# Kernel optimization log

Hardware: AMD Instinct MI355X
Metric: run time of the kernel (lower is better)

## Reference

```python
import jax, jax.numpy as jnp
import numpy as np

B, S, D, H = 2, 2048, 1024, 16
HD = D // H  # 64
ROPE_BASE = 10000.0


def setup_inputs() -> dict:
    key = jax.random.key(0)
    k1, k2, k3 = jax.random.split(key, 3)
    std = 1.0 / np.sqrt(D)
    x = jax.random.normal(k1, (B, S, D), dtype=jnp.float32)
    w_in = jax.random.normal(k2, (3 * D, D), dtype=jnp.float32) * std
    w_out = jax.random.normal(k3, (D, D), dtype=jnp.float32) * (std / np.sqrt(2.0))
    return {"x": x, "w_in": w_in, "w_out": w_out}


def _rope_cos_sin(seq_len, head_dim):
    inv_freq = 1.0 / (ROPE_BASE ** (jnp.arange(0, head_dim, 2, dtype=jnp.float32) / head_dim))
    t = jnp.arange(seq_len, dtype=jnp.float32)
    freqs = jnp.einsum("s,d->sd", t, inv_freq)          # [S, HD/2]
    emb = jnp.concatenate([freqs, freqs], axis=-1)       # [S, HD]
    return jnp.cos(emb)[None, :, None, :], jnp.sin(emb)[None, :, None, :]


def _rotate_half(x):
    x1, x2 = jnp.split(x, 2, axis=-1)
    return jnp.concatenate([-x2, x1], axis=-1)


def _apply_rope(x, cos, sin):
    return x * cos + _rotate_half(x) * sin


def reference(x, w_in, w_out):
    b, s, d = x.shape
    # fused QKV projection (no bias)
    qkv = x @ w_in.T                                      # [B, S, 3D]
    q, k, v = jnp.split(qkv, 3, axis=-1)
    q = q.reshape(b, s, H, HD)
    k = k.reshape(b, s, H, HD)
    v = v.reshape(b, s, H, HD)
    # rotary (offset = 0, no KV cache)
    cos, sin = _rope_cos_sin(s, HD)
    q = _apply_rope(q, cos, sin)
    k = _apply_rope(k, cos, sin)
    # causal SDPA, scale 1/sqrt(head_dim)
    scale = 1.0 / jnp.sqrt(jnp.asarray(HD, dtype=x.dtype))
    scores = jnp.einsum("bqhd,bkhd->bhqk", q, k) * scale  # [B, H, S, S]
    causal = jnp.tril(jnp.ones((s, s), dtype=bool))
    scores = jnp.where(causal, scores, jnp.asarray(-jnp.inf, dtype=scores.dtype))
    attn = jax.nn.softmax(scores, axis=-1)
    out = jnp.einsum("bhqk,bkhd->bqhd", attn, v).reshape(b, s, d)
    return out @ w_out.T
```

## Files before the change

kernel.cpp:

```cpp
#include <hip/hip_runtime.h>
#include <hip/hip_bf16.h>
#include <math.h>

#define NB 2
#define NS 2048
#define ND 1024
#define NH 16
#define HD 64
#define BS (NB*NS)
#define D3 (3*ND)
#define NT (NS/64)

typedef __bf16 bf16;
typedef __bf16 bf16x4 __attribute__((ext_vector_type(4)));
typedef __bf16 bf16x8 __attribute__((ext_vector_type(8)));
typedef float f32x4 __attribute__((ext_vector_type(4)));

#define MFMA16(a,b,c) __builtin_amdgcn_mfma_f32_16x16x32_bf16(a,b,c,0,0,0)

static __device__ inline f32x4 zero4() { f32x4 z; z[0]=0.f; z[1]=0.f; z[2]=0.f; z[3]=0.f; return z; }

__device__ __forceinline__ void gload_lds16(const bf16* g, bf16* l) {
    __builtin_amdgcn_global_load_lds(
        (__attribute__((address_space(1))) unsigned int*)g,
        (__attribute__((address_space(3))) unsigned int*)l, 16, 0, 0);
}

#define CVT1 (BS*ND/8)
#define CVT2 (D3*ND/8)
#define CVT3 (ND*ND/8)
#define CVTN (CVT1+CVT2+CVT3)
__global__ __launch_bounds__(256) void prep(
    const float* __restrict__ x, const float* __restrict__ w_in, const float* __restrict__ w_out,
    bf16* __restrict__ xb, bf16* __restrict__ winb, bf16* __restrict__ woutb,
    float* __restrict__ cosT, float* __restrict__ sinT)
{
    int i = blockIdx.x * 256 + threadIdx.x;
    if (i < CVTN) {
        const float* in; bf16* out; int j;
        if (i < CVT1)            { in = x;     out = xb;    j = i; }
        else if (i < CVT1+CVT2)  { in = w_in;  out = winb;  j = i - CVT1; }
        else                     { in = w_out; out = woutb; j = i - CVT1 - CVT2; }
        const float4* p = (const float4*)in;
        float4 a = p[j*2], b = p[j*2+1];
        bf16x8 o;
        o[0]=(bf16)a.x; o[1]=(bf16)a.y; o[2]=(bf16)a.z; o[3]=(bf16)a.w;
        o[4]=(bf16)b.x; o[5]=(bf16)b.y; o[6]=(bf16)b.z; o[7]=(bf16)b.w;
        ((bf16x8*)out)[j] = o;
    } else {
        int k = i - CVTN;
        int s = k >> 5, j = k & 31;
        float inv = __expf(-(float)j * (9.210340372f * 0.03125f));
        float ang = (float)s * inv;
        cosT[k] = cosf(ang);
        sinT[k] = sinf(ang);
    }
}

template<int EPI>
__global__ __launch_bounds__(256) void gemm_bt(
    const bf16* __restrict__ A, const bf16* __restrict__ Bm,
    float* __restrict__ C, bf16* __restrict__ Qb, bf16* __restrict__ Kb, bf16* __restrict__ Vt,
    const float* __restrict__ cosT, const float* __restrict__ sinT,
    int M, int N, int K)
{
    __shared__ bf16 As[2][128*64];
    __shared__ bf16 Bs[2][128*64];
    int t = threadIdx.x;
    int lane = t & 63, w = t >> 6;
    int wr = w >> 1, wc = w & 1;
    int lr = lane & 15, lg = lane >> 4;
    int m0 = blockIdx.y * 128, n0 = blockIdx.x * 128;

    int srow = lane >> 3;
    int schunk = (lane & 7) ^ srow;
    const bf16* gA = &A [(size_t)(m0 + w*32 + srow)*K + schunk*8];
    const bf16* gB = &Bm[(size_t)(n0 + w*32 + srow)*K + schunk*8];

    auto stage = [&](int kt) {
        int buf = kt & 1;
        bf16* lA = &As[buf][w*2048];
        bf16* lB = &Bs[buf][w*2048];
        int k0 = kt * 64;
        #pragma unroll
        for (int i=0;i<4;i++) {
            gload_lds16(gA + (size_t)(i*8)*K + k0, lA + i*512);
            gload_lds16(gB + (size_t)(i*8)*K + k0, lB + i*512);
        }
    };

    f32x4 acc[4][4];
    for (int m=0;m<4;m++) for (int n=0;n<4;n++) acc[m][n] = zero4();

    int nt = K >> 6;
    stage(0);
    stage(1);

    for (int kt = 0; kt < nt; kt++) {
        int cur = kt & 1;
        if (kt < nt-1) asm volatile("s_waitcnt vmcnt(8)" ::: "memory");
        else           asm volatile("s_waitcnt vmcnt(0)" ::: "memory");
        __builtin_amdgcn_s_barrier();
        __builtin_amdgcn_sched_barrier(0);

        bf16x8 af[2][4], bfr[2][4];
        #pragma unroll
        for (int ks=0;ks<2;ks++) {
            #pragma unroll
            for (int m=0;m<4;m++) {
                int row = wr*64 + m*16 + lr;
                af[ks][m] = *(const bf16x8*)&As[cur][row*64 + (((ks*4+lg) ^ (row&7))*8)];
            }
            #pragma unroll
            for (int n=0;n<4;n++) {
                int row = wc*64 + n*16 + lr;
                bfr[ks][n] = *(const bf16x8*)&Bs[cur][row*64 + (((ks*4+lg) ^ (row&7))*8)];
            }
        }
        asm volatile("s_waitcnt lgkmcnt(0)" ::: "memory");
        __builtin_amdgcn_sched_barrier(0);
        __builtin_amdgcn_s_barrier();
        __builtin_amdgcn_sched_barrier(0);

        if (kt + 2 < nt) stage(kt + 2);

        __builtin_amdgcn_s_setprio(1);
        #pragma unroll
        for (int ks=0;ks<2;ks++)
            #pragma unroll
            for (int m=0;m<4;m++)
                #pragma unroll
                for (int n=0;n<4;n++)
                    acc[m][n] = MFMA16(af[ks][m], bfr[ks][n], acc[m][n]);
        __builtin_amdgcn_s_setprio(0);
    }

    if (EPI == 0) {
        for (int m=0;m<4;m++) for (int n=0;n<4;n++) {
            int grow = m0 + wr*64 + m*16 + lg*4;
            int gcol = n0 + wc*64 + n*16 + lr;
            for (int r=0;r<4;r++)
                C[(size_t)(grow+r) * N + gcol] = acc[m][n][r];
        }
    } else {
        int which = n0 >> 10;
        if (which == 2) {
            for (int m=0;m<4;m++) for (int n=0;n<4;n++) {
                int grow = m0 + wr*64 + m*16 + lg*4;
                int gcol = n0 + wc*64 + n*16 + lr;
                int h = (gcol & 1023) >> 6, d = gcol & 63;
                int b = grow >> 11, s0 = grow & (NS-1);
                int shi = s0 & ~63, j = s0 & 63;
                int kp = ((j>>5)&1)*32 + ((j>>2)&3)*8 + ((j>>4)&1)*4;
                bf16x4 pv;
                for (int r=0;r<4;r++) pv[r] = (bf16)acc[m][n][r];
                *(bf16x4*)&Vt[((size_t)((b*NH + h)*HD + d))*NS + shi + kp] = pv;
            }
        } else {
            const float qs = 0.125f * 1.44269504f;
            bf16* dst = (which == 0) ? Qb : Kb;
            for (int m=0;m<4;m++) {
                int grow = m0 + wr*64 + m*16 + lg*4;
                #pragma unroll
                for (int n=0;n<2;n++) {
                    int gcol = n0 + wc*64 + n*16 + lr;
                    int h = (gcol & 1023) >> 6, j = gcol & 63;
                    #pragma unroll
                    for (int r=0;r<4;r++) {
                        int gm = grow + r;
                        int b = gm >> 11, s = gm & (NS-1);
                        float c  = cosT[(s<<5)+j];
                        float sn = sinT[(s<<5)+j];
                        float x1 = acc[m][n][r], x2 = acc[m][n+2][r];
                        float y1 = x1*c - x2*sn;
                        float y2 = x2*c + x1*sn;
                        if (which == 0) { y1 *= qs; y2 *= qs; }
                        size_t off = ((size_t)((b*NH + h)*NS + s))*HD;
                        dst[off + j]      = (bf16)y1;
                        dst[off + j + 32] = (bf16)y2;
                    }
                }
            }
        }
    }
}

__global__ __launch_bounds__(256, 4) void attn_fwd(
    const bf16* __restrict__ Qb, const bf16* __restrict__ Kb, const bf16* __restrict__ Vp,
    bf16* __restrict__ AO)
{
    __shared__ bf16 Ks[2][64*64];
    __shared__ bf16 Vs[2][64*64];
    int t = threadIdx.x;
    int lane = t & 63, w = t >> 6;
    int lr = lane & 15, lg = lane >> 4;
    int wgid = blockIdx.x;
    int qt = (NT-1) - (wgid >> 5);
    int bh = wgid & 31;
    int b = bh >> 4, h = bh & 15;
    size_t base = (size_t)bh * NS * HD;
    int q0 = qt*64 + w*16;

    bf16x8 qf[2];
    #pragma unroll
    for (int c=0;c<2;c++)
        qf[c] = *(const bf16x8*)&Qb[base + (size_t)(q0+lr)*HD + c*32 + lg*8];

    float m_r = -__builtin_inff(), l_r = 0.f;
    f32x4 o[4];
    #pragma unroll
    for (int n=0;n<4;n++) o[n] = zero4();

    int srow = t >> 3;
    int sch  = t & 7;
    int sslot = sch ^ (srow & 7);
    bf16x8 kr[2], vr[2];

    auto load_window = [&](int kv0) {
        #pragma unroll
        for (int i=0;i<2;i++)
            kr[i] = *(const bf16x8*)&Kb[base + (size_t)(kv0 + i*32 + srow)*HD + sch*8];
        #pragma unroll
        for (int i=0;i<2;i++)
            vr[i] = *(const bf16x8*)&Vp[base + (size_t)(i*32 + srow)*NS + kv0 + sch*8];
    };
    auto store_window = [&](int buf) {
        #pragma unroll
        for (int i=0;i<2;i++)
            *(bf16x8*)&Ks[buf][(i*32 + srow)*64 + sslot*8] = kr[i];
        #pragma unroll
        for (int i=0;i<2;i++)
            *(bf16x8*)&Vs[buf][(i*32 + srow)*64 + sslot*8] = vr[i];
    };

    for (int kt = 0; kt <= qt; kt++) {
        if (kt == 0) { load_window(0); store_window(0); __syncthreads(); }
        int cur = kt & 1;
        int kv0 = kt*64;
        bool last = (kt == qt);
        if (!last) load_window(kv0 + 64);

        const bf16* ksb = &Ks[cur][0];
        const bf16* vsb = &Vs[cur][0];

        f32x4 sc[4];
        __builtin_amdgcn_s_setprio(1);
        #pragma unroll
        for (int kb=0;kb<4;kb++) {
            int row = kb*16 + lr;
            bf16x8 k0 = *(const bf16x8*)&ksb[row*64 + ((lg     ^ (row&7))*8)];
            bf16x8 k1 = *(const bf16x8*)&ksb[row*64 + (((4+lg) ^ (row&7))*8)];
            sc[kb] = MFMA16(k0, qf[0], zero4());
            sc[kb] = MFMA16(k1, qf[1], sc[kb]);
        }
        __builtin_amdgcn_s_setprio(0);

        if (last) {
            int qi = q0 + lr;
            #pragma unroll
            for (int kb=0;kb<4;kb++)
                #pragma unroll
                for (int r=0;r<4;r++)
                    if (kv0 + kb*16 + lg*4 + r > qi) sc[kb][r] = -__builtin_inff();
        }

        float tm = fmaxf(fmaxf(sc[0][0],sc[0][1]), fmaxf(sc[0][2],sc[0][3]));
        #pragma unroll
        for (int kb=1;kb<4;kb++)
            tm = fmaxf(tm, fmaxf(fmaxf(sc[kb][0],sc[kb][1]), fmaxf(sc[kb][2],sc[kb][3])));
        tm = fmaxf(tm, __shfl_xor(tm, 16));
        tm = fmaxf(tm, __shfl_xor(tm, 32));
        if (!__all(tm <= m_r + 8.0f)) {
            float mn = fmaxf(m_r, tm);
            float fsc = exp2f(m_r - mn);
            l_r *= fsc;
            #pragma unroll
            for (int n=0;n<4;n++) o[n] *= fsc;
            m_r = mn;
        }
        float p[4][4];
        float ps = 0.f;
        #pragma unroll
        for (int kb=0;kb<4;kb++)
            #pragma unroll
            for (int r=0;r<4;r++) {
                float pe = exp2f(sc[kb][r] - m_r);
                p[kb][r] = pe;
                ps += pe;
            }
        ps += __shfl_xor(ps, 16);
        ps += __shfl_xor(ps, 32);
        l_r += ps;

        bf16x8 pa[2];
        #pragma unroll
        for (int c=0;c<2;c++) {
            bf16x8 v;
            #pragma unroll
            for (int i=0;i<8;i++) v[i] = (bf16)p[c*2 + (i>>2)][i&3];
            pa[c] = v;
        }

        __builtin_amdgcn_s_setprio(1);
        #pragma unroll
        for (int c=0;c<2;c++)
            #pragma unroll
            for (int n=0;n<4;n++) {
                int row = n*16 + lr;
                bf16x8 vf = *(const bf16x8*)&vsb[row*64 + (((c*4+lg) ^ (row&7))*8)];
                o[n] = MFMA16(vf, pa[c], o[n]);
            }
        __builtin_amdgcn_s_setprio(0);

        if (!last) { store_window(cur^1); __syncthreads(); }
    }

    float inv = 1.0f / l_r;
    int q = q0 + lr;
    #pragma unroll
    for (int n=0;n<4;n++) {
        bf16x4 ov;
        #pragma unroll
        for (int r=0;r<4;r++) ov[r] = (bf16)(o[n][r] * inv);
        *(bf16x4*)&AO[((size_t)(b*NS + q)*NH + h)*HD + n*16 + lg*4] = ov;
    }
}

extern "C" void kernel_launch(void* const* d_in, const int* in_sizes, int n_in,
                              void* d_out, int out_size, void* d_ws, size_t ws_size,
                              hipStream_t stream) {
    const float* x     = (const float*)d_in[0];
    const float* w_in  = (const float*)d_in[1];
    const float* w_out = (const float*)d_in[2];
    float* out = (float*)d_out;

    char* p = (char*)d_ws;
    bf16* xb    = (bf16*)p; p += (size_t)BS*ND*2;
    bf16* winb  = (bf16*)p; p += (size_t)D3*ND*2;
    bf16* woutb = (bf16*)p; p += (size_t)ND*ND*2;
    bf16* Qb    = (bf16*)p; p += (size_t)NB*NH*NS*HD*2;
    bf16* Kb    = (bf16*)p; p += (size_t)NB*NH*NS*HD*2;
    bf16* Vp    = (bf16*)p; p += (size_t)NB*NH*NS*HD*2;
    bf16* AO    = (bf16*)p; p += (size_t)BS*ND*2;
    float* cosT = (float*)p; p += (size_t)NS*32*4;
    float* sinT = (float*)p; p += (size_t)NS*32*4;

    prep<<<(CVTN + NS*32)/256, 256, 0, stream>>>(x, w_in, w_out, xb, winb, woutb, cosT, sinT);
    gemm_bt<1><<<dim3(D3/128, BS/128), 256, 0, stream>>>(xb, winb, nullptr, Qb, Kb, Vp,
                                                         cosT, sinT, BS, D3, ND);
    attn_fwd<<<NB*NH*NT, 256, 0, stream>>>(Qb, Kb, Vp, AO);
    gemm_bt<0><<<dim3(ND/128, BS/128), 256, 0, stream>>>(AO, woutb, out, nullptr, nullptr, nullptr,
                                                         nullptr, nullptr, BS, ND, ND);
}
```

Baseline: 102.5 us.

## Split long causal attention rows across two blocks with last-arriver merge

The attention kernel now splits the KV range of the 24 longest query tiles per head into two halves, each processed by a separate block (1792 blocks instead of 1024). Each half writes unnormalized partial output plus max/sum to scratch that reuses the xb buffer, and an atomic counter lets the second finisher merge both halves. This targets load imbalance and the tail from causal triangle work. It adds a flag memset, global partial traffic and fences, and raises launch bounds to 5 waves per SIMD, which may cost registers.

Result: slower. 383.6 us (+274.1%).

```diff
diff --git a/kernel.cpp b/kernel.cpp
--- a/kernel.cpp
+++ b/kernel.cpp
@@ -10,6 +10,7 @@
 #define BS (NB*NS)
 #define D3 (3*ND)
 #define NT (NS/64)
+#define ATTN_BLOCKS (32*56)
 
 typedef __bf16 bf16;
 typedef __bf16 bf16x4 __attribute__((ext_vector_type(4)));
@@ -185,18 +186,29 @@
     }
 }
 
-__global__ __launch_bounds__(256, 4) void attn_fwd(
+__global__ __launch_bounds__(256, 5) void attn_fwd(
     const bf16* __restrict__ Qb, const bf16* __restrict__ Kb, const bf16* __restrict__ Vp,
-    bf16* __restrict__ AO)
+    bf16* __restrict__ AO, bf16* __restrict__ pO, float* __restrict__ pML, int* __restrict__ flags)
 {
     __shared__ bf16 Ks[2][64*64];
     __shared__ bf16 Vs[2][64*64];
     int t = threadIdx.x;
     int lane = t & 63, w = t >> 6;
     int lr = lane & 15, lg = lane >> 4;
-    int wgid = blockIdx.x;
-    int qt = (NT-1) - (wgid >> 5);
-    int bh = wgid & 31;
+
+    int j = blockIdx.x;
+    int bh = j & 31, r = j >> 5;
+    int qt, k0t, k1t, half;
+    bool split = (r < 48);
+    if (split) {
+        qt = 31 - (r >> 1);
+        half = r & 1;
+        int hmid = (qt + 2) >> 1;
+        if (half == 0) { k0t = 0;    k1t = hmid - 1; }
+        else           { k0t = hmid; k1t = qt; }
+    } else {
+        qt = 55 - r; half = 0; k0t = 0; k1t = qt;
+    }
     int b = bh >> 4, h = bh & 15;
     size_t base = (size_t)bh * NS * HD;
     int q0 = qt*64 + w*16;
@@ -233,11 +245,11 @@
             *(bf16x8*)&Vs[buf][(i*32 + srow)*64 + sslot*8] = vr[i];
     };
 
-    for (int kt = 0; kt <= qt; kt++) {
-        if (kt == 0) { load_window(0); store_window(0); __syncthreads(); }
-        int cur = kt & 1;
+    for (int kt = k0t; kt <= k1t; kt++) {
+        int cur = (kt - k0t) & 1;
+        if (kt == k0t) { load_window(k0t*64); store_window(0); __syncthreads(); }
         int kv0 = kt*64;
-        bool last = (kt == qt);
+        bool last = (kt == k1t);
         if (!last) load_window(kv0 + 64);
 
         const bf16* ksb = &Ks[cur][0];
@@ -255,13 +267,13 @@
         }
         __builtin_amdgcn_s_setprio(0);
 
-        if (last) {
+        if (kt == qt) {
             int qi = q0 + lr;
             #pragma unroll
             for (int kb=0;kb<4;kb++)
                 #pragma unroll
-                for (int r=0;r<4;r++)
-                    if (kv0 + kb*16 + lg*4 + r > qi) sc[kb][r] = -__builtin_inff();
+                for (int rr=0;rr<4;rr++)
+                    if (kv0 + kb*16 + lg*4 + rr > qi) sc[kb][rr] = -__builtin_inff();
         }
 
         float tm = fmaxf(fmaxf(sc[0][0],sc[0][1]), fmaxf(sc[0][2],sc[0][3]));
@@ -283,9 +295,9 @@
         #pragma unroll
         for (int kb=0;kb<4;kb++)
             #pragma unroll
-            for (int r=0;r<4;r++) {
-                float pe = exp2f(sc[kb][r] - m_r);
-                p[kb][r] = pe;
+            for (int rr=0;rr<4;rr++) {
+                float pe = exp2f(sc[kb][rr] - m_r);
+                p[kb][rr] = pe;
                 ps += pe;
             }
         ps += __shfl_xor(ps, 16);
@@ -315,13 +327,58 @@
         if (!last) { store_window(cur^1); __syncthreads(); }
     }
 
-    float inv = 1.0f / l_r;
-    int q = q0 + lr;
+    int lq = w*16 + lr;
+    if (!split) {
+        float inv = 1.0f / l_r;
+        int q = qt*64 + lq;
+        #pragma unroll
+        for (int n=0;n<4;n++) {
+            bf16x4 ov;
+            #pragma unroll
+            for (int rr=0;rr<4;rr++) ov[rr] = (bf16)(o[n][rr] * inv);
+            *(bf16x4*)&AO[((size_t)(b*NS + q)*NH + h)*HD + n*16 + lg*4] = ov;
+        }
+        return;
+    }
+
+    int slot = bh*48 + (qt-8)*2 + half;
+    bf16* po = pO + (size_t)slot * 4096;
     #pragma unroll
     for (int n=0;n<4;n++) {
         bf16x4 ov;
         #pragma unroll
-        for (int r=0;r<4;r++) ov[r] = (bf16)(o[n][r] * inv);
+        for (int rr=0;rr<4;rr++) ov[rr] = (bf16)o[n][rr];
+        *(bf16x4*)&po[lq*64 + n*16 + lg*4] = ov;
+    }
+    if (lg == 0) {
+        pML[slot*128 + lq*2]     = m_r;
+        pML[slot*128 + lq*2 + 1] = l_r;
+    }
+    __threadfence();
+    __syncthreads();
+    int* sflag = (int*)&Ks[0][0];
+    if (t == 0) sflag[0] = atomicAdd(&flags[bh*24 + (qt-8)], 1);
+    __syncthreads();
+    if (sflag[0] == 0) return;
+    __threadfence();
+
+    int sib = slot ^ 1;
+    const bf16* ps2 = pO + (size_t)sib * 4096;
+    float mS = pML[sib*128 + lq*2];
+    float lS = pML[sib*128 + lq*2 + 1];
+    float mM  = fmaxf(m_r, mS);
+    float sMe = exp2f(m_r - mM);
+    float sS  = exp2f(mS  - mM);
+    float lM  = l_r*sMe + lS*sS;
+    float inv = 1.0f / lM;
+    int q = qt*64 + lq;
+    #pragma unroll
+    for (int n=0;n<4;n++) {
+        bf16x4 osv = *(const bf16x4*)&ps2[lq*64 + n*16 + lg*4];
+        bf16x4 ov;
+        #pragma unroll
+        for (int rr=0;rr<4;rr++)
+            ov[rr] = (bf16)((o[n][rr]*sMe + (float)osv[rr]*sS) * inv);
         *(bf16x4*)&AO[((size_t)(b*NS + q)*NH + h)*HD + n*16 + lg*4] = ov;
     }
 }
@@ -344,11 +401,15 @@
     bf16* AO    = (bf16*)p; p += (size_t)BS*ND*2;
     float* cosT = (float*)p; p += (size_t)NS*32*4;
     float* sinT = (float*)p; p += (size_t)NS*32*4;
-
+    float* pML  = (float*)p; p += (size_t)1536*128*4;
+    int*   flags= (int*)p;   p += 768*4;
+    bf16* pO    = xb;
+
+    hipMemsetAsync(flags, 0, 768*4, stream);
     prep<<<(CVTN + NS*32)/256, 256, 0, stream>>>(x, w_in, w_out, xb, winb, woutb, cosT, sinT);
     gemm_bt<1><<<dim3(D3/128, BS/128), 256, 0, stream>>>(xb, winb, nullptr, Qb, Kb, Vp,
                                                          cosT, sinT, BS, D3, ND);
-    attn_fwd<<<NB*NH*NT, 256, 0, stream>>>(Qb, Kb, Vp, AO);
+    attn_fwd<<<ATTN_BLOCKS, 256, 0, stream>>>(Qb, Kb, Vp, AO, pO, pML, flags);
     gemm_bt<0><<<dim3(ND/128, BS/128), 256, 0, stream>>>(AO, woutb, out, nullptr, nullptr, nullptr,
                                                          nullptr, nullptr, BS, ND, ND);
 }
```
